# Kernel tuning notes

Hardware: AMD Instinct MI355X
Metric: run time of the kernel (lower is better)

The kernel has to match this reference:

```python
import jax, jax.numpy as jnp
import numpy as np

def setup_inputs() -> dict:
    key = jax.random.key(0)
    x = jax.random.normal(key, (4, 1, 192, 224, 192), dtype=jnp.float32)
    return {"x": x}

def reference(x) -> jnp.ndarray:
    # Zero-pad each spatial dim by 1 (matches F.conv3d padding=1),
    # then take central differences: out[i] = (x[i+1] - x[i-1]) / 2.
    xp = jnp.pad(x, ((0, 0), (0, 0), (1, 1), (1, 1), (1, 1)))
    half = jnp.asarray(0.5, dtype=x.dtype)
    dz = (xp[:, :, 2:, 1:-1, 1:-1] - xp[:, :, :-2, 1:-1, 1:-1]) * half  # D axis (dZ kernel)
    dy = (xp[:, :, 1:-1, 2:, 1:-1] - xp[:, :, 1:-1, :-2, 1:-1]) * half  # H axis (dY kernel)
    dx = (xp[:, :, 1:-1, 1:-1, 2:] - xp[:, :, 1:-1, 1:-1, :-2]) * half  # W axis (dX kernel)
    return jnp.abs(dx) + jnp.abs(dy) + jnp.abs(dz)
```

## Files before the change

kernel.cpp:

```cpp
#include <hip/hip_runtime.h>


constexpr int W = 192, H = 224, D = 192, B = 4;
constexpr int W4     = W / 4;
constexpr int PLANE4 = W4 * H;
constexpr int BYP    = 4;
constexpr int ROWS   = BYP * 2;
constexpr int CHUNK  = 8;
constexpr int ZC     = D / CHUNK;
constexpr int YT     = H / ROWS;
constexpr int GRID   = B * ZC * YT;
constexpr int PERX   = GRID / 8;

__global__ __launch_bounds__(192) void grad3d_kernel(
    const float* __restrict__ in, float* __restrict__ out) {
    int bid = blockIdx.x;
    int sid = (bid & 7) * PERX + (bid >> 3);
    const int yt = sid % YT; sid /= YT;
    const int zc = sid % ZC; sid /= ZC;
    const int b  = sid;

    const int xv = threadIdx.x;
    const int tp = threadIdx.y;
    const int r0 = yt * ROWS + tp * 2;
    const int r1 = r0 + 1;
    const int z0 = zc * CHUNK;

    const float4* __restrict__ in4 = (const float4*)in;
    float4* __restrict__ out4 = (float4*)out;
    const float4 zf = make_float4(0.f, 0.f, 0.f, 0.f);

    const bool has_l  = (xv > 0);
    const bool has_r  = (xv < W4 - 1);
    const bool has_ym = (r0 > 0);
    const bool has_yp = (r1 + 1 < H);

    int base = (b * D + z0) * PLANE4 + r0 * W4 + xv;

    float4 cm0 = (z0 > 0) ? in4[base - PLANE4]      : zf;
    float4 cm1 = (z0 > 0) ? in4[base - PLANE4 + W4] : zf;
    float4 c00 = in4[base];
    float4 c01 = in4[base + W4];
    float4 cp0 = in4[base + PLANE4];
    float4 cp1 = in4[base + PLANE4 + W4];
    float4 ym  = has_ym ? in4[base - W4]     : zf;
    float4 yp  = has_yp ? in4[base + 2 * W4] : zf;
    float  l0  = has_l ? in[base * 4 - 1]        : 0.f;
    float  r0e = has_r ? in[base * 4 + 4]        : 0.f;
    float  l1  = has_l ? in[(base + W4) * 4 - 1] : 0.f;
    float  r1e = has_r ? in[(base + W4) * 4 + 4] : 0.f;

#pragma unroll
    for (int i = 0; i < CHUNK; ++i) {
        const int z  = z0 + i;
        const int nb = base + PLANE4;
        const bool vz1 = (z + 1 < D);
        const bool vz2 = (z + 2 < D);

        float4 cn0 = vz2 ? in4[nb + PLANE4]      : zf;
        float4 cn1 = vz2 ? in4[nb + PLANE4 + W4] : zf;
        float4 ymn = (vz1 && has_ym) ? in4[nb - W4]     : zf;
        float4 ypn = (vz1 && has_yp) ? in4[nb + 2 * W4] : zf;
        float  l0n = (vz1 && has_l) ? in[nb * 4 - 1]        : 0.f;
        float  r0n = (vz1 && has_r) ? in[nb * 4 + 4]        : 0.f;
        float  l1n = (vz1 && has_l) ? in[(nb + W4) * 4 - 1] : 0.f;
        float  r1n = (vz1 && has_r) ? in[(nb + W4) * 4 + 4] : 0.f;

        float4 o0, o1;
        o0.x = fabsf((c00.y - l0   ) * .5f) + fabsf((c01.x - ym.x) * .5f) + fabsf((cp0.x - cm0.x) * .5f);
        o0.y = fabsf((c00.z - c00.x) * .5f) + fabsf((c01.y - ym.y) * .5f) + fabsf((cp0.y - cm0.y) * .5f);
        o0.z = fabsf((c00.w - c00.y) * .5f) + fabsf((c01.z - ym.z) * .5f) + fabsf((cp0.z - cm0.z) * .5f);
        o0.w = fabsf((r0e  - c00.z) * .5f) + fabsf((c01.w - ym.w) * .5f) + fabsf((cp0.w - cm0.w) * .5f);
        o1.x = fabsf((c01.y - l1   ) * .5f) + fabsf((yp.x - c00.x) * .5f) + fabsf((cp1.x - cm1.x) * .5f);
        o1.y = fabsf((c01.z - c01.x) * .5f) + fabsf((yp.y - c00.y) * .5f) + fabsf((cp1.y - cm1.y) * .5f);
        o1.z = fabsf((c01.w - c01.y) * .5f) + fabsf((yp.z - c00.z) * .5f) + fabsf((cp1.z - cm1.z) * .5f);
        o1.w = fabsf((r1e  - c01.z) * .5f) + fabsf((yp.w - c00.w) * .5f) + fabsf((cp1.w - cm1.w) * .5f);
        out4[base]      = o0;
        out4[base + W4] = o1;

        cm0 = c00; cm1 = c01; c00 = cp0; c01 = cp1; cp0 = cn0; cp1 = cn1;
        ym = ymn; yp = ypn; l0 = l0n; r0e = r0n; l1 = l1n; r1e = r1n;
        base = nb;
    }
}

extern "C" void kernel_launch(void* const* d_in, const int* in_sizes, int n_in,
                              void* d_out, int out_size, void* d_ws, size_t ws_size,
                              hipStream_t stream) {
    const float* x = (const float*)d_in[0];
    float* out     = (float*)d_out;
    dim3 block(W4, BYP);
    grad3d_kernel<<<GRID, block, 0, stream>>>(x, out);
}
```

Before: 247.8 us.

## Replace z-marching register pipeline with short 2-plane chunks and nontemporal stores

Drops the 8-deep z-march that rotated planes through registers. Each thread now handles one row across two z-planes and loads the z and y neighbours directly, which creates many more blocks and more memory-level parallelism per launch. Outputs are written with nontemporal stores so the write stream stays out of cache. The trade-off is more redundant input reads (about 2 of 4 z-planes and every y-neighbour row are re-read), which relies on L2/MALL to absorb the extra traffic.

```diff
diff --git a/kernel.cpp b/kernel.cpp
--- a/kernel.cpp
+++ b/kernel.cpp
@@ -4,13 +4,14 @@
 constexpr int W = 192, H = 224, D = 192, B = 4;
 constexpr int W4     = W / 4;
 constexpr int PLANE4 = W4 * H;
-constexpr int BYP    = 4;
-constexpr int ROWS   = BYP * 2;
-constexpr int CHUNK  = 8;
-constexpr int ZC     = D / CHUNK;
-constexpr int YT     = H / ROWS;
+constexpr int BY     = 4;
+constexpr int CH     = 2;
+constexpr int ZC     = D / CH;
+constexpr int YT     = H / BY;
 constexpr int GRID   = B * ZC * YT;
 constexpr int PERX   = GRID / 8;
+
+typedef float f32x4 __attribute__((ext_vector_type(4)));
 
 __global__ __launch_bounds__(192) void grad3d_kernel(
     const float* __restrict__ in, float* __restrict__ out) {
@@ -21,67 +22,46 @@
     const int b  = sid;
 
     const int xv = threadIdx.x;
-    const int tp = threadIdx.y;
-    const int r0 = yt * ROWS + tp * 2;
-    const int r1 = r0 + 1;
-    const int z0 = zc * CHUNK;
+    const int r  = yt * BY + threadIdx.y;
+    const int z0 = zc * CH;
 
-    const float4* __restrict__ in4 = (const float4*)in;
-    float4* __restrict__ out4 = (float4*)out;
-    const float4 zf = make_float4(0.f, 0.f, 0.f, 0.f);
+    const f32x4* __restrict__ in4 = (const f32x4*)in;
+    f32x4* __restrict__ out4 = (f32x4*)out;
+    const f32x4 zf = {0.f, 0.f, 0.f, 0.f};
 
     const bool has_l  = (xv > 0);
     const bool has_r  = (xv < W4 - 1);
-    const bool has_ym = (r0 > 0);
-    const bool has_yp = (r1 + 1 < H);
+    const bool has_ym = (r > 0);
+    const bool has_yp = (r < H - 1);
 
-    int base = (b * D + z0) * PLANE4 + r0 * W4 + xv;
+    const int i0 = (b * D + z0) * PLANE4 + r * W4 + xv;
+    const int i1 = i0 + PLANE4;
 
-    float4 cm0 = (z0 > 0) ? in4[base - PLANE4]      : zf;
-    float4 cm1 = (z0 > 0) ? in4[base - PLANE4 + W4] : zf;
-    float4 c00 = in4[base];
-    float4 c01 = in4[base + W4];
-    float4 cp0 = in4[base + PLANE4];
-    float4 cp1 = in4[base + PLANE4 + W4];
-    float4 ym  = has_ym ? in4[base - W4]     : zf;
-    float4 yp  = has_yp ? in4[base + 2 * W4] : zf;
-    float  l0  = has_l ? in[base * 4 - 1]        : 0.f;
-    float  r0e = has_r ? in[base * 4 + 4]        : 0.f;
-    float  l1  = has_l ? in[(base + W4) * 4 - 1] : 0.f;
-    float  r1e = has_r ? in[(base + W4) * 4 + 4] : 0.f;
+    f32x4 czm = (z0 > 0)     ? in4[i0 - PLANE4] : zf;
+    f32x4 c0  =                in4[i0];
+    f32x4 c1  =                in4[i1];
+    f32x4 czp = (z0 + 2 < D) ? in4[i1 + PLANE4] : zf;
+    f32x4 ym0 = has_ym ? in4[i0 - W4] : zf;
+    f32x4 yp0 = has_yp ? in4[i0 + W4] : zf;
+    f32x4 ym1 = has_ym ? in4[i1 - W4] : zf;
+    f32x4 yp1 = has_yp ? in4[i1 + W4] : zf;
+    float l0  = has_l ? in[i0 * 4 - 1] : 0.f;
+    float r0e = has_r ? in[i0 * 4 + 4] : 0.f;
+    float l1  = has_l ? in[i1 * 4 - 1] : 0.f;
+    float r1e = has_r ? in[i1 * 4 + 4] : 0.f;
 
-#pragma unroll
-    for (int i = 0; i < CHUNK; ++i) {
-        const int z  = z0 + i;
-        const int nb = base + PLANE4;
-        const bool vz1 = (z + 1 < D);
-        const bool vz2 = (z + 2 < D);
+    f32x4 o0, o1;
+    o0.x = fabsf((c0.y - l0  ) * .5f) + fabsf((yp0.x - ym0.x) * .5f) + fabsf((c1.x - czm.x) * .5f);
+    o0.y = fabsf((c0.z - c0.x) * .5f) + fabsf((yp0.y - ym0.y) * .5f) + fabsf((c1.y - czm.y) * .5f);
+    o0.z = fabsf((c0.w - c0.y) * .5f) + fabsf((yp0.z - ym0.z) * .5f) + fabsf((c1.z - czm.z) * .5f);
+    o0.w = fabsf((r0e  - c0.z) * .5f) + fabsf((yp0.w - ym0.w) * .5f) + fabsf((c1.w - czm.w) * .5f);
+    o1.x = fabsf((c1.y - l1  ) * .5f) + fabsf((yp1.x - ym1.x) * .5f) + fabsf((czp.x - c0.x) * .5f);
+    o1.y = fabsf((c1.z - c1.x) * .5f) + fabsf((yp1.y - ym1.y) * .5f) + fabsf((czp.y - c0.y) * .5f);
+    o1.z = fabsf((c1.w - c1.y) * .5f) + fabsf((yp1.z - ym1.z) * .5f) + fabsf((czp.z - c0.z) * .5f);
+    o1.w = fabsf((r1e  - c1.z) * .5f) + fabsf((yp1.w - ym1.w) * .5f) + fabsf((czp.w - c0.w) * .5f);
 
-        float4 cn0 = vz2 ? in4[nb + PLANE4]      : zf;
-        float4 cn1 = vz2 ? in4[nb + PLANE4 + W4] : zf;
-        float4 ymn = (vz1 && has_ym) ? in4[nb - W4]     : zf;
-        float4 ypn = (vz1 && has_yp) ? in4[nb + 2 * W4] : zf;
-        float  l0n = (vz1 && has_l) ? in[nb * 4 - 1]        : 0.f;
-        float  r0n = (vz1 && has_r) ? in[nb * 4 + 4]        : 0.f;
-        float  l1n = (vz1 && has_l) ? in[(nb + W4) * 4 - 1] : 0.f;
-        float  r1n = (vz1 && has_r) ? in[(nb + W4) * 4 + 4] : 0.f;
-
-        float4 o0, o1;
-        o0.x = fabsf((c00.y - l0   ) * .5f) + fabsf((c01.x - ym.x) * .5f) + fabsf((cp0.x - cm0.x) * .5f);
-        o0.y = fabsf((c00.z - c00.x) * .5f) + fabsf((c01.y - ym.y) * .5f) + fabsf((cp0.y - cm0.y) * .5f);
-        o0.z = fabsf((c00.w - c00.y) * .5f) + fabsf((c01.z - ym.z) * .5f) + fabsf((cp0.z - cm0.z) * .5f);
-        o0.w = fabsf((r0e  - c00.z) * .5f) + fabsf((c01.w - ym.w) * .5f) + fabsf((cp0.w - cm0.w) * .5f);
-        o1.x = fabsf((c01.y - l1   ) * .5f) + fabsf((yp.x - c00.x) * .5f) + fabsf((cp1.x - cm1.x) * .5f);
-        o1.y = fabsf((c01.z - c01.x) * .5f) + fabsf((yp.y - c00.y) * .5f) + fabsf((cp1.y - cm1.y) * .5f);
-        o1.z = fabsf((c01.w - c01.y) * .5f) + fabsf((yp.z - c00.z) * .5f) + fabsf((cp1.z - cm1.z) * .5f);
-        o1.w = fabsf((r1e  - c01.z) * .5f) + fabsf((yp.w - c00.w) * .5f) + fabsf((cp1.w - cm1.w) * .5f);
-        out4[base]      = o0;
-        out4[base + W4] = o1;
-
-        cm0 = c00; cm1 = c01; c00 = cp0; c01 = cp1; cp0 = cn0; cp1 = cn1;
-        ym = ymn; yp = ypn; l0 = l0n; r0e = r0n; l1 = l1n; r1e = r1n;
-        base = nb;
-    }
+    __builtin_nontemporal_store(o0, out4 + i0);
+    __builtin_nontemporal_store(o1, out4 + i1);
 }
 
 extern "C" void kernel_launch(void* const* d_in, const int* in_sizes, int n_in,
@@ -89,6 +69,6 @@
                               hipStream_t stream) {
     const float* x = (const float*)d_in[0];
     float* out     = (float*)d_out;
-    dim3 block(W4, BYP);
+    dim3 block(W4, BY);
     grad3d_kernel<<<GRID, block, 0, stream>>>(x, out);
 }
```

Measured after the change: 242.1 us. 2.3% less time.
